# Kernel optimization log

Measured on AMD Instinct MI355X. Metric: run time of the kernel, lower is better.

## Reference

```python
import jax, jax.numpy as jnp
import numpy as np

NUM_CLASSES = 2
KS = 5  # kernel_size
EPS = 1e-8  # torch cosine_similarity eps


def setup_inputs() -> dict:
    key = jax.random.key(0)
    k1, k2, k3 = jax.random.split(key, 3)
    b, c, h, w = 8, 256, 128, 128
    er_input = jax.random.normal(k1, (b, c, h, w), dtype=jnp.float32)
    seg_label = jax.random.randint(k2, (b, h, w), 0, 2, dtype=jnp.int32)
    gt_boundary_seg = jax.random.randint(k3, (b, h, w), 0, 2, dtype=jnp.int32)
    return {"er_input": er_input, "seg_label": seg_label, "gt_boundary_seg": gt_boundary_seg}


def _context_loss(er_input, seg_label, gt_boundary_seg):
    # seg_label / gt_boundary_seg already at er_input spatial size (nearest interp is identity)
    b, c, h, w = er_input.shape
    r = KS // 2
    seg0 = jnp.where(seg_label == 255, 0, seg_label)
    gtb0 = jnp.where(gt_boundary_seg == 255, 0, gt_boundary_seg)
    gt_b = gtb0 * seg0                                  # [b,h,w] boundary pixels on fg classes
    interior = jnp.zeros((h, w), bool).at[r:h - r, r:w - r].set(True)
    valid = (gt_b > 0) & interior                       # pixels whose 5x5 window is in-bounds
    include = (gt_b > 0).any(axis=(1, 2))               # images contributing to scale_num
    cnt = valid.sum(axis=(1, 2)).astype(er_input.dtype)  # [b]

    norm = jnp.maximum(jnp.sqrt((er_input * er_input).sum(axis=1)), EPS)  # [b,h,w]
    validf = valid.astype(er_input.dtype)
    total = jnp.zeros((b,), dtype=er_input.dtype)
    n_shift = 0
    for dy in range(-r, r + 1):
        for dx in range(-r, r + 1):
            if dy == 0 and dx == 0:
                continue
            n_shift += 1
            # value at p+ (dy,dx) brought to p; valid pixels are interior so no wrap issue
            feat_s = jnp.roll(er_input, (-dy, -dx), axis=(2, 3))
            norm_s = jnp.roll(norm, (-dy, -dx), axis=(1, 2))
            seg_s = jnp.roll(seg_label, (-dy, -dx), axis=(1, 2))
            dot = (er_input * feat_s).sum(axis=1)       # [b,h,w]
            cos = dot / (norm * norm_s)
            # one_hot(seg,256)[:num_classes] dot product == labels equal AND label < num_classes
            labsim = ((seg_label == seg_s) & (seg_label < NUM_CLASSES)).astype(er_input.dtype)
            sq = (cos - labsim) ** 2
            # mse_loss over selected boundary pixels of image i
            total = total + (sq * validf).sum(axis=(1, 2)) / jnp.maximum(cnt, 1.0)
    loss_i = total / float(n_shift)                     # per-image context_loss_pi / 24
    scale_num = jnp.maximum(include.sum(), 1)
    return (loss_i * include.astype(loss_i.dtype)).sum() / scale_num.astype(loss_i.dtype)


def reference(er_input, seg_label, gt_boundary_seg):
    return _context_loss(er_input, seg_label, gt_boundary_seg)
```

## Files before the change

### kernel.cpp

```cpp
#include <hip/hip_runtime.h>
#include <math.h>

#define BATCH 8
#define CH    256
#define H     128
#define W     128
#define PLANE (H * W)
#define NPIX  (BATCH * PLANE)
#define NSHIFT 12
#define NMAPS  13
#define NCHUNK 4
#define CPC    (CH / NCHUNK)
#define CSTRIDE (NMAPS * NPIX)

static __device__ __constant__ int S_DY[NSHIFT] = {0,0,1,1,1,1,1,2,2,2,2,2};
static __device__ __constant__ int S_DX[NSHIFT] = {1,2,-2,-1,0,1,2,-2,-1,0,1,2};

#define TROWS  16
#define SROWS  (TROWS + 2)
#define NTILE  (H / TROWS)
#define NCORRB (BATCH * NTILE * NCHUNK)

__device__ __forceinline__ void fma4(float& acc, const float4& a, const float4& b) {
    acc = fmaf(a.x, b.x, acc);
    acc = fmaf(a.y, b.y, acc);
    acc = fmaf(a.z, b.z, acc);
    acc = fmaf(a.w, b.w, acc);
}

__global__ __launch_bounds__(64) void k_prep(int* __restrict__ cnt,
                                             int* __restrict__ inc,
                                             float* __restrict__ tot) {
    int t = threadIdx.x;
    if (t < 8) { cnt[t] = 0; inc[t] = 0; tot[t] = 0.0f; }
}

__global__ __launch_bounds__(1024, 4) void k_corr(const float* __restrict__ er,
                                                  float* __restrict__ comb) {
    __shared__ float4 lds[2][SROWS][132];
    int t = threadIdx.x;

    int blk = blockIdx.x;
    int chunk = blk & 3;
    int tile  = (blk >> 2) & 7;
    int b     = blk >> 5;
    int y0 = tile * TROWS;
    int c0 = chunk * CPC;
    int r = t >> 7;
    int x = t & 127;

    if (t < 2 * SROWS * 4) {
        int bi = t / (SROWS * 4), rem = t % (SROWS * 4);
        int row = rem >> 2, col = rem & 3;
        int xs = (col < 2) ? col : (col + 128);
        lds[bi][row][xs] = make_float4(0.f, 0.f, 0.f, 0.f);
    }

    float accA[13], accB[13];
#pragma unroll
    for (int i = 0; i < 13; i++) { accA[i] = 0.0f; accB[i] = 0.0f; }

    const float* base = er + (size_t)b * CH * PLANE;

    float pf[3][4];
    auto load_quad = [&](int c) {
#pragma unroll
        for (int k = 0; k < 3; ++k) {
            if (k < 2 || t < 256) {
                int s = t + k * 1024;
                int row = s >> 7;
                int xs = s & 127;
                int y = y0 + row;
                if (y < H) {
                    const float* p0 = base + (size_t)c * PLANE + y * W + xs;
                    pf[k][0] = p0[0];
                    pf[k][1] = p0[PLANE];
                    pf[k][2] = p0[2 * PLANE];
                    pf[k][3] = p0[3 * PLANE];
                } else {
                    pf[k][0] = 0.f; pf[k][1] = 0.f; pf[k][2] = 0.f; pf[k][3] = 0.f;
                }
            }
        }
    };
    auto commit_quad = [&](int bi) {
#pragma unroll
        for (int k = 0; k < 3; ++k) {
            if (k < 2 || t < 256) {
                int s = t + k * 1024;
                int row = s >> 7;
                int xs = s & 127;
                lds[bi][row][xs + 2] = make_float4(pf[k][0], pf[k][1], pf[k][2], pf[k][3]);
            }
        }
    };

    const int iters = CPC / 4;
    load_quad(c0);
    commit_quad(0);
    load_quad(c0 + 4);

    auto iter = [&](int it, int cur) {
        __syncthreads();
        if (it + 1 < iters) commit_quad(cur ^ 1);
        if (it + 2 < iters) load_quad(c0 + 4 * (it + 2));

        const float4* lp = &lds[cur][2 * r][x + 2];
        float4 cA = lp[0];
        float4 cB = lp[132];
        {
            float4 v1 = lp[1], v2 = lp[2];
            fma4(accA[0], cA, cA);
            fma4(accA[1], cA, v1);
            fma4(accA[2], cA, v2);
        }
        {
            float4 m2 = lp[130], m1 = lp[131], p1 = lp[133], p2 = lp[134];
            fma4(accA[3], cA, m2);
            fma4(accA[4], cA, m1);
            fma4(accA[5], cA, cB);
            fma4(accA[6], cA, p1);
            fma4(accA[7], cA, p2);
            fma4(accB[0], cB, cB);
            fma4(accB[1], cB, p1);
            fma4(accB[2], cB, p2);
        }
        {
            float4 m2 = lp[262], m1 = lp[263], v0 = lp[264], p1 = lp[265], p2 = lp[266];
            fma4(accA[8],  cA, m2);
            fma4(accA[9],  cA, m1);
            fma4(accA[10], cA, v0);
            fma4(accA[11], cA, p1);
            fma4(accA[12], cA, p2);
            fma4(accB[3], cB, m2);
            fma4(accB[4], cB, m1);
            fma4(accB[5], cB, v0);
            fma4(accB[6], cB, p1);
            fma4(accB[7], cB, p2);
        }
        {
            float4 m2 = lp[394], m1 = lp[395], v0 = lp[396], p1 = lp[397], p2 = lp[398];
            fma4(accB[8],  cB, m2);
            fma4(accB[9],  cB, m1);
            fma4(accB[10], cB, v0);
            fma4(accB[11], cB, p1);
            fma4(accB[12], cB, p2);
        }
    };

    for (int it = 0; it < iters; it += 2) {
        iter(it, 0);
        iter(it + 1, 1);
    }

    float* cb = comb + (size_t)chunk * CSTRIDE;
    int pixA = b * PLANE + (y0 + 2 * r) * W + x;
    int pixB = pixA + W;
#pragma unroll
    for (int m = 0; m < NSHIFT; ++m) {
        cb[m * NPIX + pixA] = accA[m + 1];
        cb[m * NPIX + pixB] = accB[m + 1];
    }
    cb[NSHIFT * NPIX + pixA] = accA[0];
    cb[NSHIFT * NPIX + pixB] = accB[0];
}

__global__ __launch_bounds__(256) void k_rn(const float* __restrict__ comb,
                                            float* __restrict__ rn) {
    int idx = blockIdx.x * 256 + threadIdx.x;
    const float* ns = comb + NSHIFT * NPIX;
    float s = (ns[idx] + ns[idx + CSTRIDE]) + (ns[idx + 2 * CSTRIDE] + ns[idx + 3 * CSTRIDE]);
    rn[idx] = fminf(rsqrtf(s), 1e8f);
}

__device__ __forceinline__ float sum4c(const float* __restrict__ p) {
    return (p[0] + p[CSTRIDE]) + (p[2 * CSTRIDE] + p[3 * CSTRIDE]);
}

__global__ __launch_bounds__(256) void k_loss(const float* __restrict__ comb,
                                              const float* __restrict__ rn,
                                              const int* __restrict__ seg,
                                              const int* __restrict__ gtb,
                                              int* __restrict__ cnt,
                                              int* __restrict__ inc,
                                              float* __restrict__ tot) {
    const float* dots = comb;
    int idx = blockIdx.x * 256 + threadIdx.x;
    int b = idx >> 14;
    int rem = idx & (PLANE - 1);
    int y = rem >> 7;
    int x = rem & 127;

    float val = 0.0f;
    int my_cnt = 0, my_any = 0;
    {
        int sp = seg[idx];
        int gp = gtb[idx];
        int s0 = (sp == 255) ? 0 : sp;
        int g0 = (gp == 255) ? 0 : gp;
        if (s0 > 0 && g0 > 0) {
            my_any = 1;
            if (y >= 2 && y < H - 2 && x >= 2 && x < W - 2) {
                my_cnt = 1;
                float npr = rn[idx];
                float sum = 0.0f;
#pragma unroll
                for (int i = 0; i < NSHIFT; ++i) {
                    int off = S_DY[i] * W + S_DX[i];
                    {
                        float d  = sum4c(dots + i * NPIX + idx);
                        float cosv = d * (npr * rn[idx + off]);
                        int sq = seg[idx + off];
                        float lab = (sp == sq && sp < 2) ? 1.0f : 0.0f;
                        float tt = cosv - lab;
                        sum = fmaf(tt, tt, sum);
                    }
                    {
                        float d  = sum4c(dots + i * NPIX + idx - off);
                        float cosv = d * (npr * rn[idx - off]);
                        int sq = seg[idx - off];
                        float lab = (sp == sq && sp < 2) ? 1.0f : 0.0f;
                        float tt = cosv - lab;
                        sum = fmaf(tt, tt, sum);
                    }
                }
                val = sum;
            }
        }
    }

    for (int o = 32; o > 0; o >>= 1) {
        val    += __shfl_down(val, o, 64);
        my_cnt += __shfl_down(my_cnt, o, 64);
        my_any |= __shfl_down(my_any, o, 64);
    }
    __shared__ float wsum[4];
    __shared__ int wc[4], wa[4];
    int lane = threadIdx.x & 63;
    int wid  = threadIdx.x >> 6;
    if (lane == 0) { wsum[wid] = val; wc[wid] = my_cnt; wa[wid] = my_any; }
    __syncthreads();
    if (threadIdx.x == 0) {
        float s = wsum[0] + wsum[1] + wsum[2] + wsum[3];
        int c = wc[0] + wc[1] + wc[2] + wc[3];
        int a = wa[0] | wa[1] | wa[2] | wa[3];
        if (s != 0.0f) atomicAdd(&tot[b], s);
        if (c) atomicAdd(&cnt[b], c);
        if (a) atomicOr(&inc[b], 1);
    }
}

__global__ __launch_bounds__(64) void k_fin(const int* __restrict__ cnt,
                                            const int* __restrict__ inc,
                                            const float* __restrict__ tot,
                                            float* __restrict__ out) {
    if (threadIdx.x == 0) {
        int sn = 0;
        float s = 0.0f;
#pragma unroll
        for (int b = 0; b < BATCH; ++b) {
            int ib = inc[b];
            sn += (ib != 0);
            int cb = cnt[b]; if (cb < 1) cb = 1;
            if (ib) s += tot[b] / (24.0f * (float)cb);
        }
        if (sn < 1) sn = 1;
        out[0] = s / (float)sn;
    }
}

extern "C" void kernel_launch(void* const* d_in, const int* in_sizes, int n_in,
                              void* d_out, int out_size, void* d_ws, size_t ws_size,
                              hipStream_t stream) {
    const float* er  = (const float*)d_in[0];
    const int*   seg = (const int*)d_in[1];
    const int*   gtb = (const int*)d_in[2];
    float* out = (float*)d_out;

    float* ws   = (float*)d_ws;
    float* comb = ws;
    float* rn   = comb + NCHUNK * CSTRIDE;
    float* tot  = rn + NPIX;
    int*   cnt  = (int*)(tot + 8);
    int*   inc  = cnt + 8;

    hipLaunchKernelGGL(k_prep, dim3(1), dim3(64), 0, stream, cnt, inc, tot);
    hipLaunchKernelGGL(k_corr, dim3(NCORRB), dim3(1024), 0, stream, er, comb);
    hipLaunchKernelGGL(k_rn, dim3(NPIX / 256), dim3(256), 0, stream, comb, rn);
    hipLaunchKernelGGL(k_loss, dim3(NPIX / 256), dim3(256), 0, stream,
                       comb, rn, seg, gtb, cnt, inc, tot);
    hipLaunchKernelGGL(k_fin, dim3(1), dim3(64), 0, stream, cnt, inc, tot, out);
}
```

Before: 223.4 us.

## Halve correlation tile height and fold prep/finalize kernels into neighbors

Tile rows per correlation block drop from 16 to 8 and threads per block from 1024 to 512, which doubles the block count to improve scheduling across CUs. The zeroing kernel is merged into block 0 of k_corr. The finalize kernel is replaced by a last-block-done atomic counter at the end of k_loss. This removes two kernel launches. In exchange, the halo overhead per tile rises, since 10 rows are loaded for 8 output rows instead of 18 for 16, and the correctness of the reductions now depends on fences and the counter.

```diff
diff --git a/kernel.cpp b/kernel.cpp
--- a/kernel.cpp
+++ b/kernel.cpp
@@ -16,10 +16,11 @@
 static __device__ __constant__ int S_DY[NSHIFT] = {0,0,1,1,1,1,1,2,2,2,2,2};
 static __device__ __constant__ int S_DX[NSHIFT] = {1,2,-2,-1,0,1,2,-2,-1,0,1,2};
 
-#define TROWS  16
+#define TROWS  8
 #define SROWS  (TROWS + 2)
 #define NTILE  (H / TROWS)
 #define NCORRB (BATCH * NTILE * NCHUNK)
+#define NLOSSB (NPIX / 256)
 
 __device__ __forceinline__ void fma4(float& acc, const float4& a, const float4& b) {
     acc = fmaf(a.x, b.x, acc);
@@ -28,29 +29,34 @@
     acc = fmaf(a.w, b.w, acc);
 }
 
-__global__ __launch_bounds__(64) void k_prep(int* __restrict__ cnt,
-                                             int* __restrict__ inc,
-                                             float* __restrict__ tot) {
-    int t = threadIdx.x;
-    if (t < 8) { cnt[t] = 0; inc[t] = 0; tot[t] = 0.0f; }
-}
-
-__global__ __launch_bounds__(1024, 4) void k_corr(const float* __restrict__ er,
-                                                  float* __restrict__ comb) {
+__global__ __launch_bounds__(512, 4) void k_corr(const float* __restrict__ er,
+                                                 float* __restrict__ comb,
+                                                 int* __restrict__ cnt,
+                                                 int* __restrict__ inc,
+                                                 float* __restrict__ tot,
+                                                 unsigned int* __restrict__ done) {
     __shared__ float4 lds[2][SROWS][132];
     int t = threadIdx.x;
 
+    if (blockIdx.x == 0) {
+        if (t < 8)               cnt[t] = 0;
+        else if (t < 16)         inc[t - 8] = 0;
+        else if (t < 24)         tot[t - 16] = 0.0f;
+        else if (t == 24)        *done = 0u;
+    }
+
     int blk = blockIdx.x;
     int chunk = blk & 3;
-    int tile  = (blk >> 2) & 7;
-    int b     = blk >> 5;
+    int tile  = (blk >> 2) & 15;
+    int b     = blk >> 6;
     int y0 = tile * TROWS;
     int c0 = chunk * CPC;
     int r = t >> 7;
     int x = t & 127;
 
-    if (t < 2 * SROWS * 4) {
-        int bi = t / (SROWS * 4), rem = t % (SROWS * 4);
+    if (t >= 128 && t < 128 + 2 * SROWS * 4) {
+        int u = t - 128;
+        int bi = u / (SROWS * 4), rem = u % (SROWS * 4);
         int row = rem >> 2, col = rem & 3;
         int xs = (col < 2) ? col : (col + 128);
         lds[bi][row][xs] = make_float4(0.f, 0.f, 0.f, 0.f);
@@ -67,7 +73,7 @@
 #pragma unroll
         for (int k = 0; k < 3; ++k) {
             if (k < 2 || t < 256) {
-                int s = t + k * 1024;
+                int s = t + k * 512;
                 int row = s >> 7;
                 int xs = s & 127;
                 int y = y0 + row;
@@ -87,7 +93,7 @@
 #pragma unroll
         for (int k = 0; k < 3; ++k) {
             if (k < 2 || t < 256) {
-                int s = t + k * 1024;
+                int s = t + k * 512;
                 int row = s >> 7;
                 int xs = s & 127;
                 lds[bi][row][xs + 2] = make_float4(pf[k][0], pf[k][1], pf[k][2], pf[k][3]);
@@ -183,7 +189,9 @@
                                               const int* __restrict__ gtb,
                                               int* __restrict__ cnt,
                                               int* __restrict__ inc,
-                                              float* __restrict__ tot) {
+                                              float* __restrict__ tot,
+                                              unsigned int* __restrict__ done,
+                                              float* __restrict__ out) {
     const float* dots = comb;
     int idx = blockIdx.x * 256 + threadIdx.x;
     int b = idx >> 14;
@@ -247,25 +255,22 @@
         if (s != 0.0f) atomicAdd(&tot[b], s);
         if (c) atomicAdd(&cnt[b], c);
         if (a) atomicOr(&inc[b], 1);
-    }
-}
-
-__global__ __launch_bounds__(64) void k_fin(const int* __restrict__ cnt,
-                                            const int* __restrict__ inc,
-                                            const float* __restrict__ tot,
-                                            float* __restrict__ out) {
-    if (threadIdx.x == 0) {
-        int sn = 0;
-        float s = 0.0f;
-#pragma unroll
-        for (int b = 0; b < BATCH; ++b) {
-            int ib = inc[b];
-            sn += (ib != 0);
-            int cb = cnt[b]; if (cb < 1) cb = 1;
-            if (ib) s += tot[b] / (24.0f * (float)cb);
-        }
-        if (sn < 1) sn = 1;
-        out[0] = s / (float)sn;
+        __threadfence();
+        unsigned int old = atomicAdd(done, 1u);
+        if (old == NLOSSB - 1) {
+            __threadfence();
+            int sn = 0;
+            float fs = 0.0f;
+#pragma unroll
+            for (int b2 = 0; b2 < BATCH; ++b2) {
+                int ib = inc[b2];
+                sn += (ib != 0);
+                int cb = cnt[b2]; if (cb < 1) cb = 1;
+                if (ib) fs += tot[b2] / (24.0f * (float)cb);
+            }
+            if (sn < 1) sn = 1;
+            out[0] = fs / (float)sn;
+        }
     }
 }
 
@@ -283,11 +288,11 @@
     float* tot  = rn + NPIX;
     int*   cnt  = (int*)(tot + 8);
     int*   inc  = cnt + 8;
-
-    hipLaunchKernelGGL(k_prep, dim3(1), dim3(64), 0, stream, cnt, inc, tot);
-    hipLaunchKernelGGL(k_corr, dim3(NCORRB), dim3(1024), 0, stream, er, comb);
+    unsigned int* done = (unsigned int*)(inc + 8);
+
+    hipLaunchKernelGGL(k_corr, dim3(NCORRB), dim3(512), 0, stream,
+                       er, comb, cnt, inc, tot, done);
     hipLaunchKernelGGL(k_rn, dim3(NPIX / 256), dim3(256), 0, stream, comb, rn);
-    hipLaunchKernelGGL(k_loss, dim3(NPIX / 256), dim3(256), 0, stream,
-                       comb, rn, seg, gtb, cnt, inc, tot);
-    hipLaunchKernelGGL(k_fin, dim3(1), dim3(64), 0, stream, cnt, inc, tot, out);
-}
+    hipLaunchKernelGGL(k_loss, dim3(NLOSSB), dim3(256), 0, stream,
+                       comb, rn, seg, gtb, cnt, inc, tot, done, out);
+}
```

Measured after the change: 225.5 us. Within noise of the previous version (+1.0%).
